# Optimization experiments

Hardware: AMD Instinct MI355X
Metric: run time of the kernel (lower is better)

Reference implementation:

```python
import jax, jax.numpy as jnp
import numpy as np
import math

DIM = 1024      # dim == dim_attn (required by value-reshape)
HEAD = 16
KV = 128        # K_v routing slots
HD = DIM // HEAD
N = 50000       # number of nodes


def setup_inputs() -> dict:
    key = jax.random.key(0)
    ks = jax.random.split(key, 8)
    s = lambda fan_in: 1.0 / np.sqrt(fan_in)
    return {
        "x": jax.random.normal(ks[0], (N, DIM), jnp.float32),
        "node_index": jax.random.normal(ks[1], (N, 4), jnp.float32),
        # nn.Linear(dim, dim_attn)
        "Wq": jax.random.normal(ks[2], (DIM, DIM), jnp.float32) * s(DIM),
        "bq": jnp.zeros((DIM,), jnp.float32),
        # nn.Parameter key (K_v, head, head_dim), torch.randn init
        "key_p": jax.random.normal(ks[3], (KV, HEAD, HD), jnp.float32),
        # nn.Linear(dim, dim)
        "Wv": jax.random.normal(ks[4], (DIM, DIM), jnp.float32) * s(DIM),
        "bv": jnp.zeros((DIM,), jnp.float32),
        # gate params, shape (head, 1)
        "alpha": jnp.full((HEAD, 1), math.log(9.0), jnp.float32),
        "beta": jnp.full((HEAD, 1), math.log(0.01), jnp.float32),
        # nn.Linear(4, head*K_v)
        "Wb": jax.random.normal(ks[5], (HEAD * KV, 4), jnp.float32) * s(4),
        "bb": jnp.zeros((HEAD * KV,), jnp.float32),
    }


def _mh_sinkhorn(A, num_iters=3, eps=0.05):
    # A: (N, H, K). Faithful to the per-head torch sinkhorn (Q transposed to
    # (K, N)): row sums are over the node axis, col sums over the slot axis.
    n = A.shape[0]
    k = A.shape[2]
    Q = jnp.exp(A / eps)
    Q = Q / jnp.sum(Q, axis=(0, 2), keepdims=True)          # total-sum norm per head
    for _ in range(num_iters):
        Q = Q / jnp.sum(Q, axis=0, keepdims=True) / k       # rows of Q.T (per slot)
        Q = Q / jnp.sum(Q, axis=2, keepdims=True) / n       # cols of Q.T (per node)
    return Q * n


def reference(x, node_index, Wq, bq, key_p, Wv, bv, alpha, beta, Wb, bb):
    n = x.shape[0]
    q = (x @ Wq.T + bq).reshape(n, HEAD, HD)
    attn = jnp.einsum('nhd,rhd->nhr', q, key_p) / np.float32(np.sqrt(HD))
    bias = (node_index @ Wb.T + bb).reshape(n, HEAD, KV)
    attn = attn + bias                                       # (n, H, K_v)
    xv = (x @ Wv.T + bv).reshape(n, HEAD, HD)
    v = jnp.einsum('nhr,nhd->rhd', jax.nn.sigmoid(attn), xv)  # (K_v, H, D)
    cons = _mh_sinkhorn(jax.nn.softmax(attn, axis=-1))
    v = jnp.einsum('nhr,rhd->nhd', cons, v)
    out = jax.nn.sigmoid(alpha) * xv + jax.nn.sigmoid(beta) * v  # (H,1) broadcasts
    return out.reshape(n, DIM)
```

## Files before the change

### kernel.cpp

```cpp
#include <hip/hip_runtime.h>

#define N_NODES 50000
#define MPAD    50176
#define DIM     1024
#define HEAD    16
#define KV      128
#define HD      64
#define NGRP    98

typedef unsigned short ushort_t;
typedef short short8 __attribute__((ext_vector_type(8)));
typedef float f32x4 __attribute__((ext_vector_type(4)));

__device__ inline unsigned short f2bf(float f){
  union { float f; unsigned u; } v; v.f = f;
  unsigned u = v.u;
  unsigned r = (u + 0x7FFFu + ((u >> 16) & 1u)) >> 16;
  return (unsigned short)r;
}
__device__ inline float bf2f(unsigned u16){
  union { unsigned u; float f; } v; v.u = (u16 & 0xFFFFu) << 16; return v.f;
}

__device__ inline void gload_lds16(const void* g, void* l){
  __builtin_amdgcn_global_load_lds(
      (const __attribute__((address_space(1))) void*)g,
      (__attribute__((address_space(3))) void*)l, 16, 0, 0);
}

__device__ inline short8 frag64(const ushort_t* lds, int row, int kk, int lane){
  int c  = kk*4 + (lane >> 4);
  int cc = c ^ (row & 7);
  return *(const short8*)(lds + row*64 + cc*8);
}
__device__ inline short8 frag128(const ushort_t* lds, int row, int kk, int lane){
  int c  = kk*4 + (lane >> 4);
  int cc = c ^ (row & 7);
  return *(const short8*)(lds + row*128 + cc*8);
}

__global__ void k_zero(float* p, int n){
  int i = blockIdx.x*256 + threadIdx.x;
  if (i < n) p[i] = 0.f;
}

__global__ void k_prep_x(const float* __restrict__ x, ushort_t* __restrict__ x_bf){
  int idx = blockIdx.x*256 + threadIdx.x;
  int row = idx >> 7, c = idx & 127;
  const float4* s = (const float4*)(x + (size_t)row*1024 + c*8);
  float4 f0 = s[0], f1 = s[1];
  short8 v;
  v[0]=(short)f2bf(f0.x); v[1]=(short)f2bf(f0.y); v[2]=(short)f2bf(f0.z); v[3]=(short)f2bf(f0.w);
  v[4]=(short)f2bf(f1.x); v[5]=(short)f2bf(f1.y); v[6]=(short)f2bf(f1.z); v[7]=(short)f2bf(f1.w);
  int sc = (c & ~7) | ((c ^ row) & 7);
  *(short8*)(x_bf + (size_t)row*1024 + sc*8) = v;
}

__global__ void k_prep_w(const float* __restrict__ Wq, const float* __restrict__ Wv,
                         ushort_t* __restrict__ w_bf){
  int idx = blockIdx.x*256 + threadIdx.x;
  int j = idx >> 10, k = idx & 1023;
  float v = (j < 1024) ? Wq[idx] : Wv[(size_t)(j-1024)*1024 + k];
  int d = k & 63;
  int scol = (k & ~63) | ((((d>>3) ^ (j & 7)) & 7) << 3) | (d & 7);
  w_bf[(size_t)j*1024 + scol] = f2bf(v);
}

__global__ void k_prep_key(const float* __restrict__ key_p, ushort_t* __restrict__ key_bf){
  int idx = blockIdx.x*256 + threadIdx.x;
  int h = idx >> 13, rem = idx & 8191;
  int r = rem >> 6, d = rem & 63;
  float v = key_p[(size_t)(r*HEAD + h)*HD + d];
  int pos = ((((d>>3) ^ (r & 7)) & 7) << 3) | (d & 7);
  key_bf[(size_t)h*8192 + r*64 + pos] = f2bf(v);
}

__global__ void k_vreduce(const float* __restrict__ vp, float* __restrict__ vout){
  int i = blockIdx.x*256 + threadIdx.x;
  float s = 0.f;
  for (int gg = 0; gg < NGRP; ++gg) s += vp[(size_t)gg*131072 + i];
  vout[i] = s;
}

__global__ __launch_bounds__(512) void k_gemm(const ushort_t* __restrict__ x_bf,
    const ushort_t* __restrict__ w_bf, const float* __restrict__ bq,
    const float* __restrict__ bv, ushort_t* __restrict__ q_bf, float* xv_out){
  extern __shared__ char gsm[];
  ushort_t* As = (ushort_t*)gsm;
  ushort_t* Bs = (ushort_t*)(gsm + 65536);
  const int tid = threadIdx.x, lane = tid & 63;
  const int wid = tid >> 6, wr = wid >> 2, wc = wid & 3;
  int b = blockIdx.x;
  int wg = (b & 7)*196 + (b >> 3);
  const int bm0 = (wg >> 3) * 256, bn0 = (wg & 7) * 256;

  f32x4 acc[8][4];
  #pragma unroll
  for (int m=0;m<8;m++)
    #pragma unroll
    for (int n=0;n<4;n++) acc[m][n] = (f32x4){0.f,0.f,0.f,0.f};

  const ushort_t* asrc = x_bf + (size_t)bm0*1024;
  const ushort_t* bsrc = w_bf + (size_t)bn0*1024;

#define STAGE(kt, bi)                                                    \
  { _Pragma("unroll")                                                    \
    for (int it=0; it<4; ++it){                                          \
      int chunk = it*512 + tid;                                          \
      int r = chunk >> 3, c = chunk & 7;                                 \
      gload_lds16(asrc + (size_t)r*1024 + (kt)*64 + c*8,                 \
                  As + (bi)*16384 + chunk*8);                            \
    }                                                                    \
    _Pragma("unroll")                                                    \
    for (int it=0; it<4; ++it){                                          \
      int chunk = it*512 + tid;                                          \
      int r = chunk >> 3, c = chunk & 7;                                 \
      gload_lds16(bsrc + (size_t)r*1024 + (kt)*64 + c*8,                 \
                  Bs + (bi)*16384 + chunk*8);                            \
    }                                                                    \
  }

  STAGE(0, 0);
  STAGE(1, 1);

  for (int kt = 0; kt < 16; ++kt){
    const int cur = kt & 1;
    if (kt == 15) { asm volatile("s_waitcnt vmcnt(0)" ::: "memory"); }
    else          { asm volatile("s_waitcnt vmcnt(8)" ::: "memory"); }
    __builtin_amdgcn_s_barrier();

    const ushort_t* ab  = As + cur*16384;
    const ushort_t* bb_ = Bs + cur*16384;
    #pragma unroll
    for (int kk=0;kk<2;kk++){
      short8 bfr[4];
      #pragma unroll
      for (int n=0;n<4;n++) bfr[n] = frag64(bb_, wc*64 + n*16 + (lane&15), kk, lane);
      #pragma unroll
      for (int m=0;m<8;m++){
        short8 af = frag64(ab, wr*128 + m*16 + (lane&15), kk, lane);
        #pragma unroll
        for (int n=0;n<4;n++)
          acc[m][n] = __builtin_amdgcn_mfma_f32_16x16x32_bf16(af, bfr[n], acc[m][n], 0,0,0);
      }
    }
    __builtin_amdgcn_s_barrier();
    if (kt + 2 < 16) STAGE(kt+2, cur);
  }
#undef STAGE

  __syncthreads();

  const bool isq = bn0 < 1024;
  float biasv[4];
  #pragma unroll
  for (int n=0;n<4;n++){
    int col = bn0 + wc*64 + n*16 + (lane & 15);
    biasv[n] = isq ? bq[col] : bv[col - 1024];
  }

  if (isq){
    ushort_t* img = (ushort_t*)gsm;
    #pragma unroll
    for (int n=0;n<4;n++){
      int lcol = wc*64 + n*16 + (lane & 15);
      int d = lcol & 63;
      #pragma unroll
      for (int m=0;m<8;m++){
        #pragma unroll
        for (int j=0;j<4;j++){
          int lrow = wr*128 + m*16 + (lane>>4)*4 + j;
          int sc = (lcol & ~63) | ((((d>>3) ^ (lrow & 7)) & 7) << 3) | (d & 7);
          img[lrow*256 + sc] = f2bf(acc[m][n][j] + biasv[n]);
        }
      }
    }
    __syncthreads();
    #pragma unroll
    for (int it=0; it<16; ++it){
      int r  = it*16 + (tid >> 5);
      int ch = tid & 31;
      short8 v = *(const short8*)(img + r*256 + ch*8);
      *(short8*)(q_bf + (size_t)(bm0 + r)*1024 + bn0 + ch*8) = v;
    }
  } else {
    #pragma unroll
    for (int n=0;n<4;n++){
      int col = bn0 + wc*64 + n*16 + (lane & 15);
      #pragma unroll
      for (int m=0;m<8;m++){
        #pragma unroll
        for (int j=0;j<4;j++){
          int row = bm0 + wr*128 + m*16 + (lane>>4)*4 + j;
          if (row < N_NODES)
            xv_out[(size_t)row*1024 + (col - 1024)] = acc[m][n][j] + biasv[n];
        }
      }
    }
  }
}

__global__ __launch_bounds__(256) void k_s1(const ushort_t* __restrict__ q_bf,
    const ushort_t* __restrict__ key_bf, const float* __restrict__ ni,
    const float* __restrict__ Wb, const float* __restrict__ bb,
    const float* __restrict__ cs_in, float* __restrict__ cs_out){
  __shared__ float col_acc[4][128];
  const int tid = threadIdx.x, lane = tid & 63, wid = tid >> 6;
  const int h   = blockIdx.x & 15;
  const int blk = blockIdx.x >> 4;
  const int gw  = blk*4 + wid;
  const int cl  = lane & 15, rg = lane >> 4;

  float wbv[8][4], bbr[8], wv[8];
  #pragma unroll
  for (int n=0;n<8;n++){
    int r = h*128 + n*16 + cl;
    float4 w4 = *(const float4*)(Wb + (size_t)r*4);
    wbv[n][0]=w4.x; wbv[n][1]=w4.y; wbv[n][2]=w4.z; wbv[n][3]=w4.w;
    bbr[n] = bb[r];
    wv[n]  = 1.f/(128.f*cs_in[r]);
  }
  short8 kf[8][2];
  #pragma unroll
  for (int n=0;n<8;n++)
    #pragma unroll
    for (int kk=0;kk<2;kk++){
      int c = (kk*4+rg) ^ (cl & 7);
      kf[n][kk] = *(const short8*)(key_bf + (size_t)h*8192 + (n*16+cl)*64 + c*8);
    }

  float cs_acc[8];
  #pragma unroll
  for (int n=0;n<8;n++) cs_acc[n] = 0.f;

  const int g0 = gw*8;
  short8 qc[2], qn[2];
  { int row = g0*16 + cl;
    #pragma unroll
    for (int kk=0;kk<2;kk++){
      int c = (kk*4+rg) ^ (row & 7);
      qc[kk] = *(const short8*)(q_bf + (size_t)row*1024 + h*64 + c*8);
    } }

  for (int u = 0; u < 8; ++u){
    const int i0 = (g0+u)*16;
    if (u+1 < 8){
      int row = i0 + 16 + cl;
      #pragma unroll
      for (int kk=0;kk<2;kk++){
        int c = (kk*4+rg) ^ (row & 7);
        qn[kk] = *(const short8*)(q_bf + (size_t)row*1024 + h*64 + c*8);
      }
    }
    float4 ni4[4];
    #pragma unroll
    for (int j=0;j<4;j++){
      int row = i0 + rg*4 + j;
      if (row < N_NODES) ni4[j] = *(const float4*)(ni + (size_t)row*4);
      else { ni4[j].x=0.f; ni4[j].y=0.f; ni4[j].z=0.f; ni4[j].w=0.f; }
    }
    f32x4 acc[8];
    #pragma unroll
    for (int n=0;n<8;n++) acc[n] = (f32x4){0.f,0.f,0.f,0.f};
    #pragma unroll
    for (int n=0;n<8;n++){
      acc[n] = __builtin_amdgcn_mfma_f32_16x16x32_bf16(qc[0], kf[n][0], acc[n], 0,0,0);
      acc[n] = __builtin_amdgcn_mfma_f32_16x16x32_bf16(qc[1], kf[n][1], acc[n], 0,0,0);
    }
    float a[8][4];
    #pragma unroll
    for (int n=0;n<8;n++)
      #pragma unroll
      for (int j=0;j<4;j++)
        a[n][j] = acc[n][j]*0.125f
                + wbv[n][0]*ni4[j].x + wbv[n][1]*ni4[j].y
                + wbv[n][2]*ni4[j].z + wbv[n][3]*ni4[j].w + bbr[n];

    float mj[4], sj[4];
    #pragma unroll
    for (int j=0;j<4;j++){
      float m0 = a[0][j];
      #pragma unroll
      for (int n=1;n<8;n++) m0 = fmaxf(m0, a[n][j]);
      m0 = fmaxf(m0, __shfl_xor(m0,1));
      m0 = fmaxf(m0, __shfl_xor(m0,2));
      m0 = fmaxf(m0, __shfl_xor(m0,4));
      m0 = fmaxf(m0, __shfl_xor(m0,8));
      mj[j] = m0;
    }
    #pragma unroll
    for (int j=0;j<4;j++){
      float s = 0.f;
      #pragma unroll
      for (int n=0;n<8;n++){ float e = __expf(a[n][j]-mj[j]); a[n][j]=e; s+=e; }
      s += __shfl_xor(s,1); s += __shfl_xor(s,2);
      s += __shfl_xor(s,4); s += __shfl_xor(s,8);
      sj[j] = s;
    }
    #pragma unroll
    for (int j=0;j<4;j++){
      float inv = 20.f/sj[j];
      #pragma unroll
      for (int n=0;n<8;n++) a[n][j] = __expf(a[n][j]*inv);
    }
    float uj[4];
    #pragma unroll
    for (int j=0;j<4;j++){
      float s = 0.f;
      #pragma unroll
      for (int n=0;n<8;n++) s += a[n][j]*wv[n];
      s += __shfl_xor(s,1); s += __shfl_xor(s,2);
      s += __shfl_xor(s,4); s += __shfl_xor(s,8);
      int row = i0 + rg*4 + j;
      uj[j] = (row < N_NODES) ? 1.f/(50000.f*s) : 0.f;
    }
    #pragma unroll
    for (int n=0;n<8;n++)
      cs_acc[n] += a[n][0]*uj[0] + a[n][1]*uj[1] + a[n][2]*uj[2] + a[n][3]*uj[3];

    qc[0] = qn[0]; qc[1] = qn[1];
  }

  #pragma unroll
  for (int n=0;n<8;n++){
    float v = cs_acc[n];
    v += __shfl_xor(v,16); v += __shfl_xor(v,32);
    cs_acc[n] = v;
  }
  if (rg == 0){
    #pragma unroll
    for (int n=0;n<8;n++) col_acc[wid][n*16+cl] = cs_acc[n];
  }
  __syncthreads();
  if (tid < 128)
    atomicAdd(&cs_out[h*128+tid],
      col_acc[0][tid]+col_acc[1][tid]+col_acc[2][tid]+col_acc[3][tid]);
}

template<int PHASE>
__global__ __launch_bounds__(256) void k_attn(
    const ushort_t* __restrict__ q_bf, const ushort_t* __restrict__ key_bf,
    const float* __restrict__ node_index, const float* __restrict__ Wb,
    const float* __restrict__ bb, const float* __restrict__ colsum_in,
    float* __restrict__ colsum_out, const float* __restrict__ v_fin,
    float* __restrict__ v_part, float* xv_out,
    const float* __restrict__ alpha, const float* __restrict__ beta)
{
  constexpr int QB    = (PHASE == 2) ? 1 : 2;
  constexpr int O_Q   = 0;
  constexpr int O_KEY = O_Q + QB*8192;
  constexpr int O_NI  = O_KEY + 16384;
  constexpr int O_WB  = O_NI + QB*1024;
  constexpr int O_RED = O_WB + 2560;
  constexpr int O_COL = O_RED + 2048;
  constexpr int O_W   = O_COL + 512;
  constexpr int O_X1  = O_W + 512;
  constexpr int O_X2  = O_X1 + 16384;

  extern __shared__ char smem[];
  ushort_t* q_lds   = (ushort_t*)(smem + O_Q);
  ushort_t* key_lds = (ushort_t*)(smem + O_KEY);
  float* ni_lds  = (float*)(smem + O_NI);
  float* wb_lds  = (float*)(smem + O_WB);
  float* red_lds = (float*)(smem + O_RED);
  float* col_acc = (float*)(smem + O_COL);
  float* w_lds   = (float*)(smem + O_W);
  ushort_t* sigT     = (ushort_t*)(smem + O_X1);
  ushort_t* xvT      = (ushort_t*)(smem + O_X2);
  ushort_t* vT       = (ushort_t*)(smem + O_X1);
  ushort_t* cons_lds = (ushort_t*)(smem + O_X2);
  float*    out_lds  = (float*)(smem + O_X2);

  const int tid = threadIdx.x, lane = tid & 63, wid = tid >> 6;
  const int h    = blockIdx.x & 15;
  const int g    = blockIdx.x >> 4;
  const int base = g * 512;
  int NT = (MPAD - base) >> 6; if (NT > 8) NT = 8;

  #pragma unroll
  for (int it = 0; it < 4; ++it){
    int chunk = it*256 + tid;
    gload_lds16(key_bf + (size_t)h*8192 + chunk*8, key_lds + chunk*8);
  }
  #pragma unroll
  for (int it = 0; it < 2; ++it){
    int chunk = it*256 + tid;
    int r = chunk >> 3, c = chunk & 7;
    gload_lds16(q_bf + (size_t)(base + r)*1024 + h*64 + c*8, q_lds + chunk*8);
  }
  { int r = tid >> 2, c = tid & 3;
    ni_lds[tid] = (base + r < N_NODES) ? node_index[(size_t)(base + r)*4 + c] : 0.f; }
  if (tid < 128){
    #pragma unroll
    for (int c=0;c<4;c++) wb_lds[tid*5+c] = Wb[(size_t)(h*128 + tid)*4 + c];
    wb_lds[tid*5+4] = bb[h*128 + tid];
    if (PHASE >= 1) w_lds[tid] = 1.f / (128.f * colsum_in[h*128 + tid]);
    if (PHASE <= 1) col_acc[tid] = 0.f;
  }
  if constexpr (PHASE == 2){
    int r = tid >> 1, dh = (tid & 1)*32;
    #pragma unroll
    for (int i=0;i<32;i++){
      int d = dh + i;
      vT[d*128 + ((r>>3) ^ (d&7))*8 + (r&7)] = f2bf(v_fin[((size_t)r*16 + h)*64 + d]);
    }
  }
  float xvr[16], xvn[16];
  if constexpr (PHASE == 0){
    int d = tid & 63, q4 = tid >> 6;
    #pragma unroll
    for (int i=0;i<16;i++){
      int row = base + q4*16 + i;
      xvr[i] = (row < N_NODES) ? xv_out[(size_t)row*1024 + h*64 + d] : 0.f;
    }
  }
  f32x4 vac[2][4];
  if constexpr (PHASE == 0)
    for (int m=0;m<2;m++) for (int n=0;n<4;n++) vac[m][n] = (f32x4){0.f,0.f,0.f,0.f};

  __syncthreads();

  for (int t = 0; t < NT; ++t){
    const int i0  = base + t*64;
    const int cur = t & 1;
    const ushort_t* qb  = q_lds  + ((QB==2) ? cur*4096 : 0);
    const float*    nib = ni_lds + ((QB==2) ? cur*256  : 0);
    float ni_next = 0.f;

    if constexpr (QB == 2){
      if (t+1 < NT){
        int i1 = i0 + 64;
        #pragma unroll
        for (int it = 0; it < 2; ++it){
          int chunk = it*256 + tid;
          int r = chunk >> 3, c = chunk & 7;
          gload_lds16(q_bf + (size_t)(i1 + r)*1024 + h*64 + c*8,
                      q_lds + (cur^1)*4096 + chunk*8);
        }
        int r = tid >> 2, c = tid & 3;
        ni_next = (i0 + 64 + r < N_NODES) ? node_index[(size_t)(i0+64+r)*4 + c] : 0.f;
      }
    } else {
      if (t+1 < NT){
        int r = tid >> 2, c = tid & 3;
        ni_next = (i0 + 64 + r < N_NODES) ? node_index[(size_t)(i0+64+r)*4 + c] : 0.f;
      }
    }
    if constexpr (PHASE == 0){
      if (t+1 < NT){
        int d = tid & 63, q4 = tid >> 6;
        #pragma unroll
        for (int i=0;i<16;i++){
          int row = i0 + 64 + q4*16 + i;
          xvn[i] = (row < N_NODES) ? xv_out[(size_t)row*1024 + h*64 + d] : 0.f;
        }
      }
    }

    f32x4 acc[2][4];
    for (int m=0;m<2;m++) for (int n=0;n<4;n++) acc[m][n] = (f32x4){0.f,0.f,0.f,0.f};
    #pragma unroll
    for (int kk = 0; kk < 2; ++kk){
      short8 kf[2];
      #pragma unroll
      for (int m=0;m<2;m++) kf[m] = frag64(key_lds, wid*32 + m*16 + (lane&15), kk, lane);
      #pragma unroll
      for (int n=0;n<4;n++){
        short8 qf = frag64(qb, n*16 + (lane&15), kk, lane);
        #pragma unroll
        for (int m=0;m<2;m++)
          acc[m][n] = __builtin_amdgcn_mfma_f32_16x16x32_bf16(kf[m], qf, acc[m][n], 0,0,0);
      }
    }

    float nif[4][4];
    #pragma unroll
    for (int n=0;n<4;n++){
      int nn = n*16 + (lane&15);
      #pragma unroll
      for (int c=0;c<4;c++) nif[n][c] = nib[nn*4+c];
    }
    float a[2][4][4];
    #pragma unroll
    for (int m=0;m<2;m++){
      #pragma unroll
      for (int j=0;j<4;j++){
        int r = wid*32 + m*16 + (lane>>4)*4 + j;
        float w0 = wb_lds[r*5+0], w1 = wb_lds[r*5+1];
        float w2 = wb_lds[r*5+2], w3 = wb_lds[r*5+3], w4 = wb_lds[r*5+4];
        #pragma unroll
        for (int n=0;n<4;n++){
          float b = w4 + w0*nif[n][0] + w1*nif[n][1] + w2*nif[n][2] + w3*nif[n][3];
          a[m][n][j] = acc[m][n][j]*0.125f + b;
        }
      }
    }

    float vmask[4];
    #pragma unroll
    for (int n=0;n<4;n++) vmask[n] = (i0 + n*16 + (lane&15) < N_NODES) ? 1.f : 0.f;

    if constexpr (PHASE == 0){
      #pragma unroll
      for (int m=0;m<2;m++) for (int n=0;n<4;n++) for (int j=0;j<4;j++){
        int r  = wid*32 + m*16 + (lane>>4)*4 + j;
        int nn = n*16 + (lane&15);
        float sg = vmask[n] / (1.f + __expf(-a[m][n][j]));
        sigT[r*64 + ((((nn>>3) ^ (r&7)) & 7) << 3) + (nn&7)] = f2bf(sg);
      }
      { int d = tid & 63, q4 = tid >> 6;
        #pragma unroll
        for (int i=0;i<16;i++){
          int nn = q4*16 + i;
          xvT[d*64 + ((((nn>>3) ^ (d&7)) & 7) << 3) + (nn&7)] = f2bf(xvr[i]);
        }
      }
    }

    float pm[4];
    #pragma unroll
    for (int n=0;n<4;n++){
      float m0 = a[0][n][0];
      #pragma unroll
      for (int m=0;m<2;m++) for (int j=0;j<4;j++) m0 = fmaxf(m0, a[m][n][j]);
      m0 = fmaxf(m0, __shfl_xor(m0, 16));
      m0 = fmaxf(m0, __shfl_xor(m0, 32));
      pm[n] = m0;
    }
    if (lane < 16){
      #pragma unroll
      for (int n=0;n<4;n++) red_lds[wid*64 + n*16 + lane] = pm[n];
    }
    __syncthreads();

    if constexpr (QB == 1){
      if (t+1 < NT){
        int i1 = i0 + 64;
        #pragma unroll
        for (int it = 0; it < 2; ++it){
          int chunk = it*256 + tid;
          int r = chunk >> 3, c = chunk & 7;
          gload_lds16(q_bf + (size_t)(i1 + r)*1024 + h*64 + c*8, q_lds + chunk*8);
        }
        ni_lds[tid] = ni_next;
      }
    }

    float mnn[4], snn[4];
    #pragma unroll
    for (int n=0;n<4;n++){
      int nn = n*16 + (lane&15);
      float m0 = red_lds[nn];
      m0 = fmaxf(m0, red_lds[64+nn]); m0 = fmaxf(m0, red_lds[128+nn]); m0 = fmaxf(m0, red_lds[192+nn]);
      mnn[n] = m0;
    }
    #pragma unroll
    for (int n=0;n<4;n++){
      float s = 0.f;
      #pragma unroll
      for (int m=0;m<2;m++) for (int j=0;j<4;j++){
        float e = __expf(a[m][n][j] - mnn[n]);
        a[m][n][j] = e; s += e;
      }
      s += __shfl_xor(s, 16); s += __shfl_xor(s, 32);
      snn[n] = s;
    }
    if (lane < 16){
      #pragma unroll
      for (int n=0;n<4;n++) red_lds[256 + wid*64 + n*16 + lane] = snn[n];
    }

    if constexpr (PHASE == 0){
      #pragma unroll
      for (int kk=0;kk<2;kk++){
        short8 sa[2];
        #pragma unroll
        for (int m=0;m<2;m++) sa[m] = frag64(sigT, wid*32 + m*16 + (lane&15), kk, lane);
        #pragma unroll
        for (int n=0;n<4;n++){
          short8 xf = frag64(xvT, n*16 + (lane&15), kk, lane);
          #pragma unroll
          for (int m=0;m<2;m++)
            vac[m][n] = __builtin_amdgcn_mfma_f32_16x16x32_bf16(sa[m], xf, vac[m][n], 0,0,0);
        }
      }
    }
    __syncthreads();

    #pragma unroll
    for (int n=0;n<4;n++){
      int nn = n*16 + (lane&15);
      snn[n] = red_lds[256+nn] + red_lds[256+64+nn] + red_lds[256+128+nn] + red_lds[256+192+nn];
    }
    #pragma unroll
    for (int n=0;n<4;n++){
      float inv = 20.f / snn[n];
      #pragma unroll
      for (int m=0;m<2;m++) for (int j=0;j<4;j++)
        a[m][n][j] = __expf(a[m][n][j] * inv);
    }

    float uval[4];
    if constexpr (PHASE >= 1){
      #pragma unroll
      for (int n=0;n<4;n++){
        float s = 0.f;
        #pragma unroll
        for (int m=0;m<2;m++){
          #pragma unroll
          for (int j=0;j<4;j++){
            int r = wid*32 + m*16 + (lane>>4)*4 + j;
            s += a[m][n][j] * w_lds[r];
          }
        }
        s += __shfl_xor(s, 16); s += __shfl_xor(s, 32);
        uval[n] = s;
      }
      if (lane < 16){
        #pragma unroll
        for (int n=0;n<4;n++) red_lds[wid*64 + n*16 + lane] = uval[n];
      }
      __syncthreads();
      #pragma unroll
      for (int n=0;n<4;n++){
        int nn = n*16 + (lane&15);
        float s = red_lds[nn] + red_lds[64+nn] + red_lds[128+nn] + red_lds[192+nn];
        uval[n] = 1.f / (50000.f * s);
      }
    }

    if constexpr (PHASE <= 1){
      float cs[2][4];
      #pragma unroll
      for (int m=0;m<2;m++){
        #pragma unroll
        for (int j=0;j<4;j++){
          float s = 0.f;
          #pragma unroll
          for (int n=0;n<4;n++){
            float tv = a[m][n][j] * vmask[n];
            if (PHASE == 1) tv *= uval[n];
            s += tv;
          }
          s += __shfl_xor(s, 1); s += __shfl_xor(s, 2);
          s += __shfl_xor(s, 4); s += __shfl_xor(s, 8);
          cs[m][j] = s;
        }
      }
      if ((lane & 15) == 0){
        #pragma unroll
        for (int m=0;m<2;m++) for (int j=0;j<4;j++){
          int r = wid*32 + m*16 + (lane>>4)*4 + j;
          col_acc[r] += cs[m][j];
        }
      }
    }

    if constexpr (PHASE == 2){
      #pragma unroll
      for (int m=0;m<2;m++) for (int n=0;n<4;n++) for (int j=0;j<4;j++){
        int r  = wid*32 + m*16 + (lane>>4)*4 + j;
        int nn = n*16 + (lane&15);
        float cv = 50000.f * uval[n] * a[m][n][j] * w_lds[r];
        cons_lds[nn*128 + ((r>>3) ^ (nn&7))*8 + (r&7)] = f2bf(cv);
      }
      __syncthreads();
      f32x4 oac[4];
      for (int n=0;n<4;n++) oac[n] = (f32x4){0.f,0.f,0.f,0.f};
      #pragma unroll
      for (int kk=0;kk<4;kk++){
        short8 va = frag128(vT, wid*16 + (lane&15), kk, lane);
        #pragma unroll
        for (int n=0;n<4;n++){
          short8 cf = frag128(cons_lds, n*16 + (lane&15), kk, lane);
          oac[n] = __builtin_amdgcn_mfma_f32_16x16x32_bf16(va, cf, oac[n], 0,0,0);
        }
      }
      __syncthreads();
      #pragma unroll
      for (int n=0;n<4;n++) for (int j=0;j<4;j++){
        int d  = wid*16 + (lane>>4)*4 + j;
        int nn = n*16 + (lane&15);
        out_lds[nn*68 + d] = oac[n][j];
      }
      __syncthreads();
      float sa = 1.f/(1.f + __expf(-alpha[h]));
      float sb = 1.f/(1.f + __expf(-beta[h]));
      int nn = tid >> 2, d0 = (tid & 3)*16;
      if (i0 + nn < N_NODES){
        #pragma unroll
        for (int gq=0; gq<4; ++gq){
          float4 vf = *(const float4*)(out_lds + nn*68 + d0 + gq*4);
          float4 xf = *(const float4*)(xv_out + (size_t)(i0+nn)*1024 + h*64 + d0 + gq*4);
          float4 o;
          o.x = sa*xf.x + sb*vf.x;
          o.y = sa*xf.y + sb*vf.y;
          o.z = sa*xf.z + sb*vf.z;
          o.w = sa*xf.w + sb*vf.w;
          *(float4*)(xv_out + (size_t)(i0+nn)*1024 + h*64 + d0 + gq*4) = o;
        }
      }
    } else {
      if (t+1 < NT && QB == 2) ni_lds[(cur^1)*256 + tid] = ni_next;
      if constexpr (PHASE == 0){
        if (t+1 < NT){
          #pragma unroll
          for (int i=0;i<16;i++) xvr[i] = xvn[i];
        }
      }
      __syncthreads();
    }
  }

  if constexpr (PHASE == 0){
    float* vdst = v_part + (size_t)g*131072;
    #pragma unroll
    for (int m=0;m<2;m++) for (int n=0;n<4;n++) for (int j=0;j<4;j++){
      int r = wid*32 + m*16 + (lane>>4)*4 + j;
      int d = n*16 + (lane&15);
      vdst[((size_t)r*16 + h)*64 + d] = vac[m][n][j];
    }
  }
  if constexpr (PHASE <= 1){
    if (tid < 128) atomicAdd(&colsum_out[h*128 + tid], col_acc[tid]);
  }
}

extern "C" void kernel_launch(void* const* d_in, const int* in_sizes, int n_in,
                              void* d_out, int out_size, void* d_ws, size_t ws_size,
                              hipStream_t stream){
  const float* x     = (const float*)d_in[0];
  const float* ni    = (const float*)d_in[1];
  const float* Wq    = (const float*)d_in[2];
  const float* bq    = (const float*)d_in[3];
  const float* keyp  = (const float*)d_in[4];
  const float* Wv    = (const float*)d_in[5];
  const float* bv    = (const float*)d_in[6];
  const float* alpha = (const float*)d_in[7];
  const float* beta  = (const float*)d_in[8];
  const float* Wb    = (const float*)d_in[9];
  const float* bb    = (const float*)d_in[10];
  float* out = (float*)d_out;

  char* ws = (char*)d_ws;
  ushort_t* x_bf   = (ushort_t*)(ws);
  float*    v_part = (float*)(ws);
  ushort_t* q_bf   = (ushort_t*)(ws + 102760448);
  ushort_t* w_bf   = (ushort_t*)(ws + 205520896);
  ushort_t* key_bf = (ushort_t*)(ws + 209715200);
  float*    v_fin  = (float*)(ws + 209977344);
  float*    cs     = (float*)(ws + 210501632);

  (void)hipFuncSetAttribute((const void*)k_gemm,
      hipFuncAttributeMaxDynamicSharedMemorySize, 131072);

  k_zero<<<dim3(24), 256, 0, stream>>>(cs, 6144);
  k_zero<<<dim3(704), 256, 0, stream>>>((float*)(x_bf + (size_t)N_NODES*1024), 90112);
  k_prep_x<<<dim3(25000), 256, 0, stream>>>(x, x_bf);
  k_prep_w<<<dim3(2048*1024/256), 256, 0, stream>>>(Wq, Wv, w_bf);
  k_prep_key<<<dim3(HEAD*KV*HD/256), 256, 0, stream>>>(keyp, key_bf);
  k_gemm<<<dim3(1568), 512, 131072, stream>>>(x_bf, w_bf, bq, bv, q_bf, out);

  dim3 ag(NGRP*16);
  k_attn<0><<<ag, 256, 65024, stream>>>(q_bf, key_bf, ni, Wb, bb, nullptr,  cs,      v_fin, v_part, out, alpha, beta);
  k_vreduce<<<dim3(512), 256, 0, stream>>>(v_part, v_fin);
  k_s1<<<dim3(1568), 256, 0, stream>>>(q_bf, key_bf, ni, Wb, bb, cs,      cs+2048);
  k_s1<<<dim3(1568), 256, 0, stream>>>(q_bf, key_bf, ni, Wb, bb, cs+2048, cs+4096);
  k_attn<2><<<ag, 256, 65024, stream>>>(q_bf, key_bf, ni, Wb, bb, cs+4096, nullptr, v_fin, v_part, out, alpha, beta);
}
```

Before: 921.5 us.

## Replace phase-2 attention block kernel with per-wave 16-node sinkhorn output kernel

```diff
diff --git a/kernel.cpp b/kernel.cpp
--- a/kernel.cpp
+++ b/kernel.cpp
@@ -337,6 +337,166 @@
       col_acc[0][tid]+col_acc[1][tid]+col_acc[2][tid]+col_acc[3][tid]);
 }
 
+__global__ __launch_bounds__(256) void k_s2(const ushort_t* __restrict__ q_bf,
+    const ushort_t* __restrict__ key_bf, const float* __restrict__ ni,
+    const float* __restrict__ Wb, const float* __restrict__ bb,
+    const float* __restrict__ cs_in, const float* __restrict__ v_fin,
+    float* xv_out, const float* __restrict__ alpha, const float* __restrict__ beta){
+  __shared__ ushort_t key_lds[128*64];
+  __shared__ ushort_t vT[64*128];
+  __shared__ ushort_t consW[4][16*128];
+  const int tid = threadIdx.x, lane = tid & 63, wid = tid >> 6;
+  const int h   = blockIdx.x & 15;
+  const int blk = blockIdx.x >> 4;
+  const int gw  = blk*4 + wid;
+  const int cl  = lane & 15, rg = lane >> 4;
+
+  #pragma unroll
+  for (int it = 0; it < 4; ++it){
+    int chunk = it*256 + tid;
+    gload_lds16(key_bf + (size_t)h*8192 + chunk*8, key_lds + chunk*8);
+  }
+  { int r = tid >> 1, dh = (tid & 1)*32;
+    #pragma unroll
+    for (int i=0;i<32;i++){
+      int d = dh + i;
+      vT[d*128 + ((r>>3) ^ (d&7))*8 + (r&7)] = f2bf(v_fin[((size_t)r*16 + h)*64 + d]);
+    } }
+
+  float wbv[8][4], bbr[8], wv[8];
+  #pragma unroll
+  for (int n=0;n<8;n++){
+    int r = h*128 + n*16 + cl;
+    float4 w4 = *(const float4*)(Wb + (size_t)r*4);
+    wbv[n][0]=w4.x; wbv[n][1]=w4.y; wbv[n][2]=w4.z; wbv[n][3]=w4.w;
+    bbr[n] = bb[r];
+    wv[n]  = 1.f/(128.f*cs_in[r]);
+  }
+  const float sa = 1.f/(1.f + __expf(-alpha[h]));
+  const float sb = 1.f/(1.f + __expf(-beta[h]));
+
+  __syncthreads();
+
+  ushort_t* cw = consW[wid];
+  const int g0 = gw*8;
+  short8 qc[2], qn[2];
+  { int row = g0*16 + cl;
+    #pragma unroll
+    for (int kk=0;kk<2;kk++){
+      int c = (kk*4+rg) ^ (row & 7);
+      qc[kk] = *(const short8*)(q_bf + (size_t)row*1024 + h*64 + c*8);
+    } }
+
+  for (int u = 0; u < 8; ++u){
+    const int i0 = (g0+u)*16;
+    if (u+1 < 8){
+      int row = i0 + 16 + cl;
+      #pragma unroll
+      for (int kk=0;kk<2;kk++){
+        int c = (kk*4+rg) ^ (row & 7);
+        qn[kk] = *(const short8*)(q_bf + (size_t)row*1024 + h*64 + c*8);
+      }
+    }
+    float4 ni4[4];
+    #pragma unroll
+    for (int j=0;j<4;j++){
+      int row = i0 + rg*4 + j;
+      if (row < N_NODES) ni4[j] = *(const float4*)(ni + (size_t)row*4);
+      else { ni4[j].x=0.f; ni4[j].y=0.f; ni4[j].z=0.f; ni4[j].w=0.f; }
+    }
+    f32x4 acc[8];
+    #pragma unroll
+    for (int n=0;n<8;n++) acc[n] = (f32x4){0.f,0.f,0.f,0.f};
+    #pragma unroll
+    for (int n=0;n<8;n++){
+      short8 k0 = frag64(key_lds, n*16+cl, 0, lane);
+      short8 k1 = frag64(key_lds, n*16+cl, 1, lane);
+      acc[n] = __builtin_amdgcn_mfma_f32_16x16x32_bf16(qc[0], k0, acc[n], 0,0,0);
+      acc[n] = __builtin_amdgcn_mfma_f32_16x16x32_bf16(qc[1], k1, acc[n], 0,0,0);
+    }
+    float a[8][4];
+    #pragma unroll
+    for (int n=0;n<8;n++)
+      #pragma unroll
+      for (int j=0;j<4;j++)
+        a[n][j] = acc[n][j]*0.125f
+                + wbv[n][0]*ni4[j].x + wbv[n][1]*ni4[j].y
+                + wbv[n][2]*ni4[j].z + wbv[n][3]*ni4[j].w + bbr[n];
+
+    float mj[4], sj[4];
+    #pragma unroll
+    for (int j=0;j<4;j++){
+      float m0 = a[0][j];
+      #pragma unroll
+      for (int n=1;n<8;n++) m0 = fmaxf(m0, a[n][j]);
+      m0 = fmaxf(m0, __shfl_xor(m0,1));
+      m0 = fmaxf(m0, __shfl_xor(m0,2));
+      m0 = fmaxf(m0, __shfl_xor(m0,4));
+      m0 = fmaxf(m0, __shfl_xor(m0,8));
+      mj[j] = m0;
+    }
+    #pragma unroll
+    for (int j=0;j<4;j++){
+      float s = 0.f;
+      #pragma unroll
+      for (int n=0;n<8;n++){ float e = __expf(a[n][j]-mj[j]); a[n][j]=e; s+=e; }
+      s += __shfl_xor(s,1); s += __shfl_xor(s,2);
+      s += __shfl_xor(s,4); s += __shfl_xor(s,8);
+      sj[j] = s;
+    }
+    #pragma unroll
+    for (int j=0;j<4;j++){
+      float inv = 20.f/sj[j];
+      #pragma unroll
+      for (int n=0;n<8;n++) a[n][j] = __expf(a[n][j]*inv);
+    }
+    float scj[4];
+    #pragma unroll
+    for (int j=0;j<4;j++){
+      float s = 0.f;
+      #pragma unroll
+      for (int n=0;n<8;n++) s += a[n][j]*wv[n];
+      s += __shfl_xor(s,1); s += __shfl_xor(s,2);
+      s += __shfl_xor(s,4); s += __shfl_xor(s,8);
+      scj[j] = 1.f/s;
+    }
+    #pragma unroll
+    for (int n=0;n<8;n++){
+      #pragma unroll
+      for (int j=0;j<4;j++){
+        int node = rg*4 + j;
+        int r = n*16 + cl;
+        int ch = (r>>3) ^ (node & 7);
+        cw[node*128 + ch*8 + (r&7)] = f2bf(scj[j]*a[n][j]*wv[n]);
+      }
+    }
+    f32x4 oac[4];
+    #pragma unroll
+    for (int nf=0;nf<4;nf++) oac[nf] = (f32x4){0.f,0.f,0.f,0.f};
+    #pragma unroll
+    for (int ks=0; ks<4; ++ks){
+      short8 ca = frag128(cw, cl, ks, lane);
+      #pragma unroll
+      for (int nf=0;nf<4;nf++){
+        short8 vb = frag128(vT, nf*16+cl, ks, lane);
+        oac[nf] = __builtin_amdgcn_mfma_f32_16x16x32_bf16(ca, vb, oac[nf], 0,0,0);
+      }
+    }
+    #pragma unroll
+    for (int j=0;j<4;j++){
+      int row = i0 + rg*4 + j;
+      if (row < N_NODES){
+        #pragma unroll
+        for (int nf=0;nf<4;nf++){
+          size_t ad = (size_t)row*1024 + h*64 + nf*16 + cl;
+          xv_out[ad] = sa*xv_out[ad] + sb*oac[nf][j];
+        }
+      }
+    }
+    qc[0] = qn[0]; qc[1] = qn[1];
+  }
+}
+
 template<int PHASE>
 __global__ __launch_bounds__(256) void k_attn(
     const ushort_t* __restrict__ q_bf, const ushort_t* __restrict__ key_bf,
@@ -346,7 +506,7 @@
     float* __restrict__ v_part, float* xv_out,
     const float* __restrict__ alpha, const float* __restrict__ beta)
 {
-  constexpr int QB    = (PHASE == 2) ? 1 : 2;
+  constexpr int QB    = 2;
   constexpr int O_Q   = 0;
   constexpr int O_KEY = O_Q + QB*8192;
   constexpr int O_NI  = O_KEY + 16384;
@@ -364,12 +524,8 @@
   float* wb_lds  = (float*)(smem + O_WB);
   float* red_lds = (float*)(smem + O_RED);
   float* col_acc = (float*)(smem + O_COL);
-  float* w_lds   = (float*)(smem + O_W);
-  ushort_t* sigT     = (ushort_t*)(smem + O_X1);
-  ushort_t* xvT      = (ushort_t*)(smem + O_X2);
-  ushort_t* vT       = (ushort_t*)(smem + O_X1);
-  ushort_t* cons_lds = (ushort_t*)(smem + O_X2);
-  float*    out_lds  = (float*)(smem + O_X2);
+  ushort_t* sigT = (ushort_t*)(smem + O_X1);
+  ushort_t* xvT  = (ushort_t*)(smem + O_X2);
 
   const int tid = threadIdx.x, lane = tid & 63, wid = tid >> 6;
   const int h    = blockIdx.x & 15;
@@ -394,66 +550,43 @@
     #pragma unroll
     for (int c=0;c<4;c++) wb_lds[tid*5+c] = Wb[(size_t)(h*128 + tid)*4 + c];
     wb_lds[tid*5+4] = bb[h*128 + tid];
-    if (PHASE >= 1) w_lds[tid] = 1.f / (128.f * colsum_in[h*128 + tid]);
-    if (PHASE <= 1) col_acc[tid] = 0.f;
-  }
-  if constexpr (PHASE == 2){
-    int r = tid >> 1, dh = (tid & 1)*32;
-    #pragma unroll
-    for (int i=0;i<32;i++){
-      int d = dh + i;
-      vT[d*128 + ((r>>3) ^ (d&7))*8 + (r&7)] = f2bf(v_fin[((size_t)r*16 + h)*64 + d]);
-    }
+    col_acc[tid] = 0.f;
   }
   float xvr[16], xvn[16];
-  if constexpr (PHASE == 0){
-    int d = tid & 63, q4 = tid >> 6;
+  { int d = tid & 63, q4 = tid >> 6;
     #pragma unroll
     for (int i=0;i<16;i++){
       int row = base + q4*16 + i;
       xvr[i] = (row < N_NODES) ? xv_out[(size_t)row*1024 + h*64 + d] : 0.f;
-    }
-  }
+    } }
   f32x4 vac[2][4];
-  if constexpr (PHASE == 0)
-    for (int m=0;m<2;m++) for (int n=0;n<4;n++) vac[m][n] = (f32x4){0.f,0.f,0.f,0.f};
+  for (int m=0;m<2;m++) for (int n=0;n<4;n++) vac[m][n] = (f32x4){0.f,0.f,0.f,0.f};
 
   __syncthreads();
 
   for (int t = 0; t < NT; ++t){
     const int i0  = base + t*64;
     const int cur = t & 1;
-    const ushort_t* qb  = q_lds  + ((QB==2) ? cur*4096 : 0);
-    const float*    nib = ni_lds + ((QB==2) ? cur*256  : 0);
+    const ushort_t* qb  = q_lds  + cur*4096;
+    const float*    nib = ni_lds + cur*256;
     float ni_next = 0.f;
 
-    if constexpr (QB == 2){
-      if (t+1 < NT){
-        int i1 = i0 + 64;
-        #pragma unroll
-        for (int it = 0; it < 2; ++it){
-          int chunk = it*256 + tid;
-          int r = chunk >> 3, c = chunk & 7;
-          gload_lds16(q_bf + (size_t)(i1 + r)*1024 + h*64 + c*8,
-                      q_lds + (cur^1)*4096 + chunk*8);
-        }
-        int r = tid >> 2, c = tid & 3;
-        ni_next = (i0 + 64 + r < N_NODES) ? node_index[(size_t)(i0+64+r)*4 + c] : 0.f;
-      }
-    } else {
-      if (t+1 < NT){
-        int r = tid >> 2, c = tid & 3;
-        ni_next = (i0 + 64 + r < N_NODES) ? node_index[(size_t)(i0+64+r)*4 + c] : 0.f;
-      }
-    }
-    if constexpr (PHASE == 0){
-      if (t+1 < NT){
-        int d = tid & 63, q4 = tid >> 6;
-        #pragma unroll
-        for (int i=0;i<16;i++){
-          int row = i0 + 64 + q4*16 + i;
-          xvn[i] = (row < N_NODES) ? xv_out[(size_t)row*1024 + h*64 + d] : 0.f;
-        }
+    if (t+1 < NT){
+      int i1 = i0 + 64;
+      #pragma unroll
+      for (int it = 0; it < 2; ++it){
+        int chunk = it*256 + tid;
+        int r = chunk >> 3, c = chunk & 7;
+        gload_lds16(q_bf + (size_t)(i1 + r)*1024 + h*64 + c*8,
+                    q_lds + (cur^1)*4096 + chunk*8);
+      }
+      int r = tid >> 2, c = tid & 3;
+      ni_next = (i0 + 64 + r < N_NODES) ? node_index[(size_t)(i0+64+r)*4 + c] : 0.f;
+      int d = tid & 63, q4 = tid >> 6;
+      #pragma unroll
+      for (int i=0;i<16;i++){
+        int row = i0 + 64 + q4*16 + i;
+        xvn[i] = (row < N_NODES) ? xv_out[(size_t)row*1024 + h*64 + d] : 0.f;
       }
     }
 
@@ -500,20 +633,18 @@
     #pragma unroll
     for (int n=0;n<4;n++) vmask[n] = (i0 + n*16 + (lane&15) < N_NODES) ? 1.f : 0.f;
 
-    if constexpr (PHASE == 0){
-      #pragma unroll
-      for (int m=0;m<2;m++) for (int n=0;n<4;n++) for (int j=0;j<4;j++){
-        int r  = wid*32 + m*16 + (lane>>4)*4 + j;
-        int nn = n*16 + (lane&15);
-        float sg = vmask[n] / (1.f + __expf(-a[m][n][j]));
-        sigT[r*64 + ((((nn>>3) ^ (r&7)) & 7) << 3) + (nn&7)] = f2bf(sg);
-      }
-      { int d = tid & 63, q4 = tid >> 6;
-        #pragma unroll
-        for (int i=0;i<16;i++){
-          int nn = q4*16 + i;
-          xvT[d*64 + ((((nn>>3) ^ (d&7)) & 7) << 3) + (nn&7)] = f2bf(xvr[i]);
-        }
+    #pragma unroll
+    for (int m=0;m<2;m++) for (int n=0;n<4;n++) for (int j=0;j<4;j++){
+      int r  = wid*32 + m*16 + (lane>>4)*4 + j;
+      int nn = n*16 + (lane&15);
+      float sg = vmask[n] / (1.f + __expf(-a[m][n][j]));
+      sigT[r*64 + ((((nn>>3) ^ (r&7)) & 7) << 3) + (nn&7)] = f2bf(sg);
+    }
+    { int d = tid & 63, q4 = tid >> 6;
+      #pragma unroll
+      for (int i=0;i<16;i++){
+        int nn = q4*16 + i;
+        xvT[d*64 + ((((nn>>3) ^ (d&7)) & 7) << 3) + (nn&7)] = f2bf(xvr[i]);
       }
     }
 
@@ -532,19 +663,6 @@
       for (int n=0;n<4;n++) red_lds[wid*64 + n*16 + lane] = pm[n];
     }
     __syncthreads();
-
-    if constexpr (QB == 1){
-      if (t+1 < NT){
-        int i1 = i0 + 64;
-        #pragma unroll
-        for (int it = 0; it < 2; ++it){
-          int chunk = it*256 + tid;
-          int r = chunk >> 3, c = chunk & 7;
-          gload_lds16(q_bf + (size_t)(i1 + r)*1024 + h*64 + c*8, q_lds + chunk*8);
-        }
-        ni_lds[tid] = ni_next;
-      }
-    }
 
     float mnn[4], snn[4];
     #pragma unroll
@@ -570,19 +688,17 @@
       for (int n=0;n<4;n++) red_lds[256 + wid*64 + n*16 + lane] = snn[n];
     }
 
-    if constexpr (PHASE == 0){
-      #pragma unroll
-      for (int kk=0;kk<2;kk++){
-        short8 sa[2];
+    #pragma unroll
+    for (int kk=0;kk<2;kk++){
+      short8 sa[2];
+      #pragma unroll
+      for (int m=0;m<2;m++) sa[m] = frag64(sigT, wid*32 + m*16 + (lane&15), kk, lane);
+      #pragma unroll
+      for (int n=0;n<4;n++){
+        short8 xf = frag64(xvT, n*16 + (lane&15), kk, lane);
         #pragma unroll
-        for (int m=0;m<2;m++) sa[m] = frag64(sigT, wid*32 + m*16 + (lane&15), kk, lane);
-        #pragma unroll
-        for (int n=0;n<4;n++){
-          short8 xf = frag64(xvT, n*16 + (lane&15), kk, lane);
-          #pragma unroll
-          for (int m=0;m<2;m++)
-            vac[m][n] = __builtin_amdgcn_mfma_f32_16x16x32_bf16(sa[m], xf, vac[m][n], 0,0,0);
-        }
+        for (int m=0;m<2;m++)
+          vac[m][n] = __builtin_amdgcn_mfma_f32_16x16x32_bf16(sa[m], xf, vac[m][n], 0,0,0);
       }
     }
     __syncthreads();
@@ -600,130 +716,43 @@
         a[m][n][j] = __expf(a[m][n][j] * inv);
     }
 
-    float uval[4];
-    if constexpr (PHASE >= 1){
-      #pragma unroll
-      for (int n=0;n<4;n++){
+    float cs[2][4];
+    #pragma unroll
+    for (int m=0;m<2;m++){
+      #pragma unroll
+      for (int j=0;j<4;j++){
         float s = 0.f;
         #pragma unroll
-        for (int m=0;m<2;m++){
-          #pragma unroll
-          for (int j=0;j<4;j++){
-            int r = wid*32 + m*16 + (lane>>4)*4 + j;
-            s += a[m][n][j] * w_lds[r];
-          }
-        }
-        s += __shfl_xor(s, 16); s += __shfl_xor(s, 32);
-        uval[n] = s;
-      }
-      if (lane < 16){
-        #pragma unroll
-        for (int n=0;n<4;n++) red_lds[wid*64 + n*16 + lane] = uval[n];
-      }
-      __syncthreads();
-      #pragma unroll
-      for (int n=0;n<4;n++){
-        int nn = n*16 + (lane&15);
-        float s = red_lds[nn] + red_lds[64+nn] + red_lds[128+nn] + red_lds[192+nn];
-        uval[n] = 1.f / (50000.f * s);
-      }
-    }
-
-    if constexpr (PHASE <= 1){
-      float cs[2][4];
-      #pragma unroll
-      for (int m=0;m<2;m++){
-        #pragma unroll
-        for (int j=0;j<4;j++){
-          float s = 0.f;
-          #pragma unroll
-          for (int n=0;n<4;n++){
-            float tv = a[m][n][j] * vmask[n];
-            if (PHASE == 1) tv *= uval[n];
-            s += tv;
-          }
-          s += __shfl_xor(s, 1); s += __shfl_xor(s, 2);
-          s += __shfl_xor(s, 4); s += __shfl_xor(s, 8);
-          cs[m][j] = s;
-        }
-      }
-      if ((lane & 15) == 0){
-        #pragma unroll
-        for (int m=0;m<2;m++) for (int j=0;j<4;j++){
-          int r = wid*32 + m*16 + (lane>>4)*4 + j;
-          col_acc[r] += cs[m][j];
-        }
-      }
-    }
-
-    if constexpr (PHASE == 2){
-      #pragma unroll
-      for (int m=0;m<2;m++) for (int n=0;n<4;n++) for (int j=0;j<4;j++){
-        int r  = wid*32 + m*16 + (lane>>4)*4 + j;
-        int nn = n*16 + (lane&15);
-        float cv = 50000.f * uval[n] * a[m][n][j] * w_lds[r];
-        cons_lds[nn*128 + ((r>>3) ^ (nn&7))*8 + (r&7)] = f2bf(cv);
-      }
-      __syncthreads();
-      f32x4 oac[4];
-      for (int n=0;n<4;n++) oac[n] = (f32x4){0.f,0.f,0.f,0.f};
-      #pragma unroll
-      for (int kk=0;kk<4;kk++){
-        short8 va = frag128(vT, wid*16 + (lane&15), kk, lane);
-        #pragma unroll
-        for (int n=0;n<4;n++){
-          short8 cf = frag128(cons_lds, n*16 + (lane&15), kk, lane);
-          oac[n] = __builtin_amdgcn_mfma_f32_16x16x32_bf16(va, cf, oac[n], 0,0,0);
-        }
-      }
-      __syncthreads();
-      #pragma unroll
-      for (int n=0;n<4;n++) for (int j=0;j<4;j++){
-        int d  = wid*16 + (lane>>4)*4 + j;
-        int nn = n*16 + (lane&15);
-        out_lds[nn*68 + d] = oac[n][j];
-      }
-      __syncthreads();
-      float sa = 1.f/(1.f + __expf(-alpha[h]));
-      float sb = 1.f/(1.f + __expf(-beta[h]));
-      int nn = tid >> 2, d0 = (tid & 3)*16;
-      if (i0 + nn < N_NODES){
-        #pragma unroll
-        for (int gq=0; gq<4; ++gq){
-          float4 vf = *(const float4*)(out_lds + nn*68 + d0 + gq*4);
-          float4 xf = *(const float4*)(xv_out + (size_t)(i0+nn)*1024 + h*64 + d0 + gq*4);
-          float4 o;
-          o.x = sa*xf.x + sb*vf.x;
-          o.y = sa*xf.y + sb*vf.y;
-          o.z = sa*xf.z + sb*vf.z;
-          o.w = sa*xf.w + sb*vf.w;
-          *(float4*)(xv_out + (size_t)(i0+nn)*1024 + h*64 + d0 + gq*4) = o;
-        }
-      }
-    } else {
-      if (t+1 < NT && QB == 2) ni_lds[(cur^1)*256 + tid] = ni_next;
-      if constexpr (PHASE == 0){
-        if (t+1 < NT){
-          #pragma unroll
-          for (int i=0;i<16;i++) xvr[i] = xvn[i];
-        }
-      }
-      __syncthreads();
-    }
-  }
-
-  if constexpr (PHASE == 0){
-    float* vdst = v_part + (size_t)g*131072;
+        for (int n=0;n<4;n++) s += a[m][n][j] * vmask[n];
+        s += __shfl_xor(s, 1); s += __shfl_xor(s, 2);
+        s += __shfl_xor(s, 4); s += __shfl_xor(s, 8);
+        cs[m][j] = s;
+      }
+    }
+    if ((lane & 15) == 0){
+      #pragma unroll
+      for (int m=0;m<2;m++) for (int j=0;j<4;j++){
+        int r = wid*32 + m*16 + (lane>>4)*4 + j;
+        col_acc[r] += cs[m][j];
+      }
+    }
+
+    if (t+1 < NT){
+      ni_lds[(cur^1)*256 + tid] = ni_next;
+      #pragma unroll
+      for (int i=0;i<16;i++) xvr[i] = xvn[i];
+    }
+    __syncthreads();
+  }
+
+  { float* vdst = v_part + (size_t)g*131072;
     #pragma unroll
     for (int m=0;m<2;m++) for (int n=0;n<4;n++) for (int j=0;j<4;j++){
       int r = wid*32 + m*16 + (lane>>4)*4 + j;
       int d = n*16 + (lane&15);
       vdst[((size_t)r*16 + h)*64 + d] = vac[m][n][j];
-    }
-  }
-  if constexpr (PHASE <= 1){
-    if (tid < 128) atomicAdd(&colsum_out[h*128 + tid], col_acc[tid]);
-  }
+    } }
+  if (tid < 128) atomicAdd(&colsum_out[h*128 + tid], col_acc[tid]);
 }
 
 extern "C" void kernel_launch(void* const* d_in, const int* in_sizes, int n_in,
@@ -762,9 +791,9 @@
   k_gemm<<<dim3(1568), 512, 131072, stream>>>(x_bf, w_bf, bq, bv, q_bf, out);
 
   dim3 ag(NGRP*16);
-  k_attn<0><<<ag, 256, 65024, stream>>>(q_bf, key_bf, ni, Wb, bb, nullptr,  cs,      v_fin, v_part, out, alpha, beta);
+  k_attn<0><<<ag, 256, 65024, stream>>>(q_bf, key_bf, ni, Wb, bb, nullptr, cs, v_fin, v_part, out, alpha, beta);
   k_vreduce<<<dim3(512), 256, 0, stream>>>(v_part, v_fin);
   k_s1<<<dim3(1568), 256, 0, stream>>>(q_bf, key_bf, ni, Wb, bb, cs,      cs+2048);
   k_s1<<<dim3(1568), 256, 0, stream>>>(q_bf, key_bf, ni, Wb, bb, cs+2048, cs+4096);
-  k_attn<2><<<ag, 256, 65024, stream>>>(q_bf, key_bf, ni, Wb, bb, cs+4096, nullptr, v_fin, v_part, out, alpha, beta);
-}
+  k_s2<<<dim3(1568), 256, 0, stream>>>(q_bf, key_bf, ni, Wb, bb, cs+4096, v_fin, out, alpha, beta);
+}
```

Result: no change. 934.8 us (+1.4%).
